# Performance work log

Measured on AMD Instinct MI355X. Metric: run time of the kernel, lower is better.

## Reference

```python
import jax, jax.numpy as jnp
import numpy as np

B, N, FD, D, H, NF, ITERS = 32, 4096, 256, 256, 4, 8, 3
DH = D // H
EPS = 1e-8
SCALE = DH ** -0.5


def layer_norm(x, g, b):
    m = x.mean(-1, keepdims=True)
    v = ((x - m) ** 2).mean(-1, keepdims=True)
    return (x - m) / jnp.sqrt(v + 1e-5) * g + b


def gru_cell(x, h, W_ih, W_hh, b_ih, b_hh):
    # PyTorch GRUCell semantics
    gi = x @ W_ih.T + b_ih  # [n, 3D]
    gh = h @ W_hh.T + b_hh
    ir, iz, inn = jnp.split(gi, 3, axis=-1)
    hr, hz, hn = jnp.split(gh, 3, axis=-1)
    r = jax.nn.sigmoid(ir + hr)
    z = jax.nn.sigmoid(iz + hz)
    n = jnp.tanh(inn + r * hn)
    return (1.0 - z) * n + z * h


def setup_inputs() -> dict:
    key = jax.random.key(0)
    ks = jax.random.split(key, 8)
    s_fd = FD ** -0.5
    s_d = D ** -0.5
    return {
        "inputs": jax.random.normal(ks[0], (B, N, FD), jnp.float32),
        "conditioning": jax.random.normal(ks[1], (B, NF, D), jnp.float32),
        "Wq": jax.random.normal(ks[2], (D, D), jnp.float32) * s_d,
        "Wk": jax.random.normal(ks[3], (D, FD), jnp.float32) * s_fd,
        "Wv": jax.random.normal(ks[4], (D, FD), jnp.float32) * s_fd,
        "W_ih": jax.random.normal(ks[5], (3 * D, D), jnp.float32) * s_d,
        "W_hh": jax.random.normal(ks[6], (3 * D, D), jnp.float32) * s_d,
        "b_ih": jnp.zeros((3 * D,), jnp.float32),
        "b_hh": jnp.zeros((3 * D,), jnp.float32),
        "ln_in_g": jnp.ones((FD,), jnp.float32),
        "ln_in_b": jnp.zeros((FD,), jnp.float32),
        "ln_f_g": jnp.ones((D,), jnp.float32),
        "ln_f_b": jnp.zeros((D,), jnp.float32),
    }


def reference(inputs, conditioning, Wq, Wk, Wv, W_ih, W_hh, b_ih, b_hh,
              ln_in_g, ln_in_b, ln_f_g, ln_f_b):
    b, n, _ = inputs.shape
    nf = conditioning.shape[1]
    x = layer_norm(inputs, ln_in_g, ln_in_b)
    k = (x @ Wk.T).reshape(b, n, H, DH)
    v = (x @ Wv.T).reshape(b, n, H, DH)

    fillers = conditioning
    attn_before = None
    for _ in range(ITERS):
        prev = fillers
        f = layer_norm(fillers, ln_f_g, ln_f_b)
        q = (f @ Wq.T).reshape(b, nf, H, DH)
        dots = jnp.einsum('bihd,bjhd->bihj', q, k) * SCALE  # [b, nf, H, n]
        # inverted softmax: over flattened (slot, head) axis
        attn = jax.nn.softmax(dots.reshape(b, nf * H, n), axis=1).reshape(b, nf, H, n)
        attn_before = attn
        a = attn + EPS
        a = a / a.sum(-1, keepdims=True)
        updates = jnp.einsum('bjhd,bihj->bihd', v, a)  # [b, nf, H, DH]
        fillers = gru_cell(updates.reshape(-1, D), prev.reshape(-1, D),
                           W_ih, W_hh, b_ih, b_hh).reshape(b, nf, D)

    # learnable_roles=False -> roles = identity, so slots == fillers
    slots = fillers
    attn_out = attn_before.mean(axis=2)  # [b, nf, n]
    return slots, attn_out
```

## Files before the change

kernel.cpp:

```cpp
#include <hip/hip_runtime.h>


#define B_ 32
#define N_ 4096
#define H_ 4
#define NF_ 8
#define SH_ 32
#define M_ (B_ * N_)
#define SCALE_ 0.125f
#define EPS_ 1e-8f

typedef __bf16 bf16x8 __attribute__((ext_vector_type(8)));
typedef float f32x4 __attribute__((ext_vector_type(4)));

__device__ __forceinline__ unsigned short f2bf(float f) {
  unsigned int u = __builtin_bit_cast(unsigned int, f);
  u += 0x7fffu + ((u >> 16) & 1u);
  return (unsigned short)(u >> 16);
}
__device__ __forceinline__ float bflo(unsigned int u) {
  return __builtin_bit_cast(float, u << 16);
}
__device__ __forceinline__ float bfhi(unsigned int u) {
  return __builtin_bit_cast(float, u & 0xffff0000u);
}
__device__ __forceinline__ float b2f(unsigned short s) {
  return __builtin_bit_cast(float, ((unsigned int)s) << 16);
}

#define GLDS16(gp, lp)                                                        \
  __builtin_amdgcn_global_load_lds(                                           \
      (const __attribute__((address_space(1))) void*)(gp),                    \
      (__attribute__((address_space(3))) void*)(lp), 16, 0, 0)

__global__ void __launch_bounds__(256) prep_kernel(
    const float* __restrict__ Wq, const float* __restrict__ Wk,
    const float* __restrict__ Wv, const float* __restrict__ Wih,
    const float* __restrict__ Whh, unsigned short* __restrict__ Bkv,
    float* __restrict__ Wqt, unsigned short* __restrict__ Wcat) {
  const int idx = blockIdx.x * 256 + threadIdx.x;
  if (idx < 131072) {
    const int n = idx >> 8, k = idx & 255;
    const float v = (n < 256) ? Wk[n * 256 + k] : Wv[(n - 256) * 256 + k];
    Bkv[idx] = f2bf(v);
  } else if (idx < 196608) {
    const int r = idx - 131072;
    const int k = r >> 8, d = r & 255;
    Wqt[r] = Wq[d * 256 + k];
  } else if (idx < 589824) {
    const int r = idx - 196608;
    const int k = r / 1536, o = r - k * 1536;
    const float v = (o < 768) ? Wih[o * 256 + k] : Whh[(o - 768) * 256 + k];
    Wcat[r] = f2bf(v);
  }
}

__global__ void __launch_bounds__(256) ln_in_kernel(
    const float* __restrict__ in, const float* __restrict__ g,
    const float* __restrict__ bb, unsigned short* __restrict__ x16) {
  const size_t row = (size_t)blockIdx.x * 4 + (threadIdx.x >> 6);
  const int lane = threadIdx.x & 63;
  const float4 xv = *(const float4*)(in + row * 256 + lane * 4);
  float s = xv.x + xv.y + xv.z + xv.w;
  float sq = xv.x * xv.x + xv.y * xv.y + xv.z * xv.z + xv.w * xv.w;
#pragma unroll
  for (int m = 1; m < 64; m <<= 1) {
    s += __shfl_xor(s, m);
    sq += __shfl_xor(sq, m);
  }
  const float mean = s * (1.f / 256.f);
  const float var = sq * (1.f / 256.f) - mean * mean;
  const float rstd = rsqrtf(var + 1e-5f);
  const float4 gv = *(const float4*)(g + lane * 4);
  const float4 bv = *(const float4*)(bb + lane * 4);
  ushort4 o;
  o.x = f2bf((xv.x - mean) * rstd * gv.x + bv.x);
  o.y = f2bf((xv.y - mean) * rstd * gv.y + bv.y);
  o.z = f2bf((xv.z - mean) * rstd * gv.z + bv.z);
  o.w = f2bf((xv.w - mean) * rstd * gv.w + bv.w);
  *(ushort4*)(x16 + row * 256 + lane * 4) = o;
}

__global__ void __launch_bounds__(256) kv_gemm(
    const unsigned short* __restrict__ x16, const unsigned short* __restrict__ Bkv,
    unsigned short* __restrict__ KV) {
  __shared__ __align__(16) unsigned short As[128 * 64];
  __shared__ __align__(16) unsigned short Bs[128 * 64];
  const int m0 = blockIdx.x * 128;
  const int n0 = blockIdx.y * 128;
  const int t = threadIdx.x;
  const int lane = t & 63, wv = t >> 6;
  const int wm = (wv & 1) * 64, wn = (wv >> 1) * 64;
  const int l15 = lane & 15, l4 = lane >> 4;
  f32x4 acc[4][4];
#pragma unroll
  for (int mi = 0; mi < 4; ++mi)
#pragma unroll
    for (int ni = 0; ni < 4; ++ni) {
      acc[mi][ni][0] = 0.f; acc[mi][ni][1] = 0.f;
      acc[mi][ni][2] = 0.f; acc[mi][ni][3] = 0.f;
    }
  const int sr = t >> 3, sc = t & 7;
  for (int kk = 0; kk < 4; ++kk) {
    const int kb = kk * 64;
#pragma unroll
    for (int i = 0; i < 4; ++i) {
      const unsigned short* ga = x16 + (size_t)(m0 + i * 32 + sr) * 256 + kb + sc * 8;
      GLDS16(ga, &As[(i * 32 + sr) * 64 + sc * 8]);
    }
#pragma unroll
    for (int i = 0; i < 4; ++i) {
      const unsigned short* gb = Bkv + (size_t)(n0 + i * 32 + sr) * 256 + kb + sc * 8;
      GLDS16(gb, &Bs[(i * 32 + sr) * 64 + sc * 8]);
    }
    asm volatile("s_waitcnt vmcnt(0)" ::: "memory");
    __syncthreads();
#pragma unroll
    for (int kc = 0; kc < 2; ++kc) {
      bf16x8 af[4], bfr[4];
#pragma unroll
      for (int mi = 0; mi < 4; ++mi)
        af[mi] = *(const bf16x8*)&As[(wm + mi * 16 + l15) * 64 + kc * 32 + l4 * 8];
#pragma unroll
      for (int ni = 0; ni < 4; ++ni)
        bfr[ni] = *(const bf16x8*)&Bs[(wn + ni * 16 + l15) * 64 + kc * 32 + l4 * 8];
#pragma unroll
      for (int mi = 0; mi < 4; ++mi)
#pragma unroll
        for (int ni = 0; ni < 4; ++ni)
          acc[mi][ni] = __builtin_amdgcn_mfma_f32_16x16x32_bf16(
              af[mi], bfr[ni], acc[mi][ni], 0, 0, 0);
    }
    __syncthreads();
  }
#pragma unroll
  for (int mi = 0; mi < 4; ++mi) {
#pragma unroll
    for (int r = 0; r < 4; ++r) {
      const int gm = m0 + wm + mi * 16 + l4 * 4 + r;
      unsigned short* dst = KV + (size_t)gm * 512 + n0 + wn + l15;
#pragma unroll
      for (int ni = 0; ni < 4; ++ni) dst[ni * 16] = f2bf(acc[mi][ni][r]);
    }
  }
}

__global__ void __launch_bounds__(256) qproj_kernel(
    const float* __restrict__ fill, const float* __restrict__ Wqt,
    const float* __restrict__ g, const float* __restrict__ bb,
    float* __restrict__ qbuf) {
  const int bi = blockIdx.x;
  const int t = threadIdx.x;
  const int wv = t >> 6, lane = t & 63;
  __shared__ float f[256];
  __shared__ float red[8];
  const float x = fill[bi * 256 + t];
  float s = x, sq = x * x;
#pragma unroll
  for (int m = 1; m < 64; m <<= 1) {
    s += __shfl_xor(s, m);
    sq += __shfl_xor(sq, m);
  }
  if (lane == 0) {
    red[wv] = s;
    red[4 + wv] = sq;
  }
  __syncthreads();
  const float S = red[0] + red[1] + red[2] + red[3];
  const float SQ = red[4] + red[5] + red[6] + red[7];
  const float mean = S * (1.f / 256.f);
  const float var = SQ * (1.f / 256.f) - mean * mean;
  const float rstd = rsqrtf(var + 1e-5f);
  f[t] = (x - mean) * rstd * g[t] + bb[t];
  __syncthreads();
  float acc = 0.f;
  for (int k = 0; k < 256; ++k) acc = fmaf(f[k], Wqt[k * 256 + t], acc);
  qbuf[(size_t)(bi * 4 + (t >> 6)) * 64 + (t & 63)] = acc;
}

__global__ void __launch_bounds__(256) attn_pass(
    const unsigned short* __restrict__ KV, const float* __restrict__ qbuf,
    float* __restrict__ partials, float* __restrict__ attn_out, int write_attn) {
  const int bid = blockIdx.x;
  const int b = bid >> 5, c = bid & 31;
  const int t = threadIdx.x;
  const int wv = t >> 6, lane = t & 63;
  const int sh = lane & 31, half = lane >> 5;
  const int h = sh & 3;

  float qr[32];
  {
    const float* qp = qbuf + (size_t)(b * 32 + sh) * 64 + half * 32;
#pragma unroll
    for (int x = 0; x < 8; ++x) {
      const float4 v = *(const float4*)(qp + x * 4);
      qr[x * 4 + 0] = v.x; qr[x * 4 + 1] = v.y;
      qr[x * 4 + 2] = v.z; qr[x * 4 + 3] = v.w;
    }
  }
  float upd[32];
#pragma unroll
  for (int x = 0; x < 32; ++x) upd[x] = 0.f;
  float ssum = 0.f;

  const int j0 = c * 128 + wv * 32;
  const unsigned short* rowp = KV + ((size_t)b * N_ + j0) * 512;

  for (int jj = 0; jj < 32; ++jj) {
    const unsigned short* kp = rowp + jj * 512 + h * 64 + half * 32;
    uint4 kw[4], vw[4];
#pragma unroll
    for (int x = 0; x < 4; ++x) kw[x] = *(const uint4*)(kp + x * 8);
#pragma unroll
    for (int x = 0; x < 4; ++x) vw[x] = *(const uint4*)(kp + 256 + x * 8);
    float dot = 0.f;
#pragma unroll
    for (int x = 0; x < 4; ++x) {
      dot = fmaf(qr[x * 8 + 0], bflo(kw[x].x), dot);
      dot = fmaf(qr[x * 8 + 1], bfhi(kw[x].x), dot);
      dot = fmaf(qr[x * 8 + 2], bflo(kw[x].y), dot);
      dot = fmaf(qr[x * 8 + 3], bfhi(kw[x].y), dot);
      dot = fmaf(qr[x * 8 + 4], bflo(kw[x].z), dot);
      dot = fmaf(qr[x * 8 + 5], bfhi(kw[x].z), dot);
      dot = fmaf(qr[x * 8 + 6], bflo(kw[x].w), dot);
      dot = fmaf(qr[x * 8 + 7], bfhi(kw[x].w), dot);
    }
    dot += __shfl_xor(dot, 32);
    const float logit = dot * SCALE_;
    float mx = logit;
#pragma unroll
    for (int m = 1; m <= 16; m <<= 1) mx = fmaxf(mx, __shfl_xor(mx, m));
    const float e = __expf(logit - mx);
    float se = e;
#pragma unroll
    for (int m = 1; m <= 16; m <<= 1) se += __shfl_xor(se, m);
    const float attn = e / se;
    ssum += attn;
#pragma unroll
    for (int x = 0; x < 4; ++x) {
      upd[x * 8 + 0] = fmaf(attn, bflo(vw[x].x), upd[x * 8 + 0]);
      upd[x * 8 + 1] = fmaf(attn, bfhi(vw[x].x), upd[x * 8 + 1]);
      upd[x * 8 + 2] = fmaf(attn, bflo(vw[x].y), upd[x * 8 + 2]);
      upd[x * 8 + 3] = fmaf(attn, bfhi(vw[x].y), upd[x * 8 + 3]);
      upd[x * 8 + 4] = fmaf(attn, bflo(vw[x].z), upd[x * 8 + 4]);
      upd[x * 8 + 5] = fmaf(attn, bfhi(vw[x].z), upd[x * 8 + 5]);
      upd[x * 8 + 6] = fmaf(attn, bflo(vw[x].w), upd[x * 8 + 6]);
      upd[x * 8 + 7] = fmaf(attn, bfhi(vw[x].w), upd[x * 8 + 7]);
    }
    if (write_attn) {
      float hs = attn;
      hs += __shfl_xor(hs, 1);
      hs += __shfl_xor(hs, 2);
      if ((lane & 3) == 0 && half == 0)
        attn_out[((size_t)b * NF_ + (sh >> 2)) * N_ + j0 + jj] = hs * 0.25f;
    }
  }

  __shared__ float uacc[SH_ * 64];
  __shared__ float sacc[SH_];
  for (int x = t; x < SH_ * 64; x += 256) uacc[x] = 0.f;
  if (t < SH_) sacc[t] = 0.f;
  __syncthreads();
  for (int w = 0; w < 4; ++w) {
    if (wv == w) {
#pragma unroll
      for (int x = 0; x < 32; ++x) uacc[sh * 64 + half * 32 + x] += upd[x];
      if (half == 0) sacc[sh] += ssum;
    }
    __syncthreads();
  }
  float* P = partials + (size_t)bid * 2080;
  for (int x = t; x < 2048; x += 256) P[x] = uacc[x];
  if (t < 32) P[2048 + t] = sacc[t];
}

__global__ void __launch_bounds__(256) gru_kernel(
    const float* __restrict__ partials, const float* __restrict__ prev,
    const unsigned short* __restrict__ Wcat, const float* __restrict__ bih,
    const float* __restrict__ bhh, float* __restrict__ out) {
  const int bi = blockIdx.x;
  const int b = bi >> 3;
  const int t = threadIdx.x;
  const int h = t >> 6;
  const int sh = (bi & 7) * 4 + h;
  __shared__ float u[256], pv[256];
  float raw = 0.f, s = 0.f;
  for (int cc = 0; cc < 32; ++cc) {
    const float* Pp = partials + (size_t)(b * 32 + cc) * 2080;
    raw += Pp[sh * 64 + (t & 63)];
    s += Pp[2048 + sh];
  }
  const float uu = raw / (s + (float)N_ * EPS_);
  u[t] = uu;
  pv[t] = prev[bi * 256 + t];
  __syncthreads();
  float a0 = bih[t], a1 = bih[256 + t], a2 = bih[512 + t];
  float a3 = bhh[t], a4 = bhh[256 + t], a5 = bhh[512 + t];
  for (int k = 0; k < 256; ++k) {
    const float uk = u[k], pk = pv[k];
    const unsigned short* wr = Wcat + k * 1536;
    a0 = fmaf(uk, b2f(wr[t]), a0);
    a1 = fmaf(uk, b2f(wr[256 + t]), a1);
    a2 = fmaf(uk, b2f(wr[512 + t]), a2);
    a3 = fmaf(pk, b2f(wr[768 + t]), a3);
    a4 = fmaf(pk, b2f(wr[1024 + t]), a4);
    a5 = fmaf(pk, b2f(wr[1280 + t]), a5);
  }
  const float r = 1.f / (1.f + __expf(-(a0 + a3)));
  const float z = 1.f / (1.f + __expf(-(a1 + a4)));
  const float n = tanhf(a2 + r * a5);
  out[bi * 256 + t] = (1.f - z) * n + z * pv[t];
}

extern "C" void kernel_launch(void* const* d_in, const int* in_sizes, int n_in,
                              void* d_out, int out_size, void* d_ws, size_t ws_size,
                              hipStream_t stream) {
  (void)in_sizes; (void)n_in; (void)out_size; (void)ws_size;
  const float* inputs = (const float*)d_in[0];
  const float* cond = (const float*)d_in[1];
  const float* Wq = (const float*)d_in[2];
  const float* Wk = (const float*)d_in[3];
  const float* Wv = (const float*)d_in[4];
  const float* Wih = (const float*)d_in[5];
  const float* Whh = (const float*)d_in[6];
  const float* bih = (const float*)d_in[7];
  const float* bhh = (const float*)d_in[8];
  const float* lng = (const float*)d_in[9];
  const float* lnb = (const float*)d_in[10];
  const float* lfg = (const float*)d_in[11];
  const float* lfb = (const float*)d_in[12];
  float* out = (float*)d_out;

  char* ws = (char*)d_ws;
  unsigned short* Bkv = (unsigned short*)(ws);
  float* Wqt = (float*)(ws + 262144);
  unsigned short* Wcat = (unsigned short*)(ws + 524288);
  unsigned short* x16 = (unsigned short*)(ws + 1310720);
  unsigned short* KV = (unsigned short*)(ws + 1310720 + 67108864);
  float* qbuf = (float*)(ws + 1310720 + 67108864 + 134217728);
  float* fillA = qbuf + 65536;
  float* fillB = fillA + 65536;
  float* partials = fillB + 65536;

  hipLaunchKernelGGL(prep_kernel, dim3(2304), dim3(256), 0, stream,
                     Wq, Wk, Wv, Wih, Whh, Bkv, Wqt, Wcat);
  hipLaunchKernelGGL(ln_in_kernel, dim3(32768), dim3(256), 0, stream,
                     inputs, lng, lnb, x16);
  hipLaunchKernelGGL(kv_gemm, dim3(1024, 4), dim3(256), 0, stream, x16, Bkv, KV);

  const float* src = cond;
  float* attn_out = out + 65536;
  for (int it = 0; it < 3; ++it) {
    float* dst = (it == 0) ? fillA : (it == 1) ? fillB : out;
    hipLaunchKernelGGL(qproj_kernel, dim3(256), dim3(256), 0, stream,
                       src, Wqt, lfg, lfb, qbuf);
    hipLaunchKernelGGL(attn_pass, dim3(1024), dim3(256), 0, stream,
                       KV, qbuf, partials, attn_out, (it == 2) ? 1 : 0);
    hipLaunchKernelGGL(gru_kernel, dim3(256), dim3(256), 0, stream,
                       partials, src, Wcat, bih, bhh, dst);
    src = dst;
  }
}
```

Before: 776.8 us.

## Compute attention logits with bf16 MFMA using head-masked block-diagonal Q

The qproj kernel now writes Q as bf16 in a zero-padded per-head layout, so each of the 32 slot-head rows spans all 256 key features. The attention pass can then compute all logits for a 32-key chunk with 16x16x32 bf16 MFMA instead of per-lane scalar dot products. Softmax over slot-heads runs on the MFMA accumulator layout, and probabilities are staged as bf16 in padded LDS before the scalar V accumulation. Q and the attention weights lose precision to bf16, and the zero padding does four times the K-dot work. The qtil and fill buffers are moved into the x16 workspace region, which is no longer read after the KV GEMM.

```diff
diff --git a/kernel.cpp b/kernel.cpp
--- a/kernel.cpp
+++ b/kernel.cpp
@@ -6,7 +6,6 @@
 #define H_ 4
 #define NF_ 8
 #define SH_ 32
-#define M_ (B_ * N_)
 #define SCALE_ 0.125f
 #define EPS_ 1e-8f
 
@@ -148,7 +147,7 @@
 __global__ void __launch_bounds__(256) qproj_kernel(
     const float* __restrict__ fill, const float* __restrict__ Wqt,
     const float* __restrict__ g, const float* __restrict__ bb,
-    float* __restrict__ qbuf) {
+    unsigned short* __restrict__ qtil) {
   const int bi = blockIdx.x;
   const int t = threadIdx.x;
   const int wv = t >> 6, lane = t & 63;
@@ -175,103 +174,141 @@
   __syncthreads();
   float acc = 0.f;
   for (int k = 0; k < 256; ++k) acc = fmaf(f[k], Wqt[k * 256 + t], acc);
-  qbuf[(size_t)(bi * 4 + (t >> 6)) * 64 + (t & 63)] = acc;
+  const int b = bi >> 3, i = bi & 7, h = t >> 6;
+  const unsigned short val = f2bf(acc);
+#pragma unroll
+  for (int hp = 0; hp < 4; ++hp)
+    qtil[(size_t)(b * 32 + i * 4 + hp) * 256 + t] = (hp == h) ? val : (unsigned short)0;
 }
 
 __global__ void __launch_bounds__(256) attn_pass(
-    const unsigned short* __restrict__ KV, const float* __restrict__ qbuf,
+    const unsigned short* __restrict__ KV, const unsigned short* __restrict__ qtil,
     float* __restrict__ partials, float* __restrict__ attn_out, int write_attn) {
   const int bid = blockIdx.x;
   const int b = bid >> 5, c = bid & 31;
   const int t = threadIdx.x;
   const int wv = t >> 6, lane = t & 63;
-  const int sh = lane & 31, half = lane >> 5;
-  const int h = sh & 3;
-
-  float qr[32];
-  {
-    const float* qp = qbuf + (size_t)(b * 32 + sh) * 64 + half * 32;
-#pragma unroll
-    for (int x = 0; x < 8; ++x) {
-      const float4 v = *(const float4*)(qp + x * 4);
-      qr[x * 4 + 0] = v.x; qr[x * 4 + 1] = v.y;
-      qr[x * 4 + 2] = v.z; qr[x * 4 + 3] = v.w;
-    }
-  }
+  const int l15 = lane & 15, lq = lane >> 4;
+  const int j0 = c * 128;
+  const int n0 = wv * 32;
+
+  __shared__ unsigned short P[32 * 130];
+  __shared__ float uacc[32 * 65];
+  __shared__ float sred[4 * 32];
+
+  f32x4 acc[2][2];
+#pragma unroll
+  for (int mt = 0; mt < 2; ++mt)
+#pragma unroll
+    for (int nt = 0; nt < 2; ++nt) {
+      acc[mt][nt][0] = 0.f; acc[mt][nt][1] = 0.f;
+      acc[mt][nt][2] = 0.f; acc[mt][nt][3] = 0.f;
+    }
+  const unsigned short* Qb = qtil + (size_t)b * 32 * 256;
+  const unsigned short* Kb = KV + ((size_t)b * N_ + j0 + n0) * 512;
+#pragma unroll
+  for (int ks = 0; ks < 8; ++ks) {
+    const bf16x8 a0 = *(const bf16x8*)(Qb + (size_t)(l15)*256 + ks * 32 + lq * 8);
+    const bf16x8 a1 = *(const bf16x8*)(Qb + (size_t)(16 + l15) * 256 + ks * 32 + lq * 8);
+#pragma unroll
+    for (int nt = 0; nt < 2; ++nt) {
+      const bf16x8 bf = *(const bf16x8*)(Kb + (size_t)(nt * 16 + l15) * 512 + ks * 32 + lq * 8);
+      acc[0][nt] = __builtin_amdgcn_mfma_f32_16x16x32_bf16(a0, bf, acc[0][nt], 0, 0, 0);
+      acc[1][nt] = __builtin_amdgcn_mfma_f32_16x16x32_bf16(a1, bf, acc[1][nt], 0, 0, 0);
+    }
+  }
+
+  float srow[8];
+#pragma unroll
+  for (int i = 0; i < 8; ++i) srow[i] = 0.f;
+#pragma unroll
+  for (int nt = 0; nt < 2; ++nt) {
+    float lv[8];
+#pragma unroll
+    for (int mt = 0; mt < 2; ++mt)
+#pragma unroll
+      for (int r = 0; r < 4; ++r) lv[mt * 4 + r] = acc[mt][nt][r] * SCALE_;
+    float mx = lv[0];
+#pragma unroll
+    for (int i = 1; i < 8; ++i) mx = fmaxf(mx, lv[i]);
+    mx = fmaxf(mx, __shfl_xor(mx, 16));
+    mx = fmaxf(mx, __shfl_xor(mx, 32));
+    float e[8];
+    float cs = 0.f;
+#pragma unroll
+    for (int i = 0; i < 8; ++i) {
+      e[i] = __expf(lv[i] - mx);
+      cs += e[i];
+    }
+    cs += __shfl_xor(cs, 16);
+    cs += __shfl_xor(cs, 32);
+    const float inv = 1.f / cs;
+    const int col = n0 + nt * 16 + l15;
+#pragma unroll
+    for (int mt = 0; mt < 2; ++mt)
+#pragma unroll
+      for (int r = 0; r < 4; ++r) {
+        const float a = e[mt * 4 + r] * inv;
+        srow[mt * 4 + r] += a;
+        P[(mt * 16 + lq * 4 + r) * 130 + col] = f2bf(a);
+      }
+    if (write_attn) {
+#pragma unroll
+      for (int mt = 0; mt < 2; ++mt) {
+        const float ao =
+            (e[mt * 4 + 0] + e[mt * 4 + 1] + e[mt * 4 + 2] + e[mt * 4 + 3]) * inv * 0.25f;
+        attn_out[((size_t)b * NF_ + mt * 4 + lq) * N_ + j0 + col] = ao;
+      }
+    }
+  }
+#pragma unroll
+  for (int k = 1; k <= 8; k <<= 1)
+#pragma unroll
+    for (int i = 0; i < 8; ++i) srow[i] += __shfl_xor(srow[i], k);
+  if (l15 == 0) {
+#pragma unroll
+    for (int mt = 0; mt < 2; ++mt)
+#pragma unroll
+      for (int r = 0; r < 4; ++r)
+        sred[wv * 32 + mt * 16 + lq * 4 + r] = srow[mt * 4 + r];
+  }
+  for (int x = t; x < 32 * 65; x += 256) uacc[x] = 0.f;
+  __syncthreads();
+
+  const int sh = lane & 31, half = lane >> 5, h = sh & 3;
   float upd[32];
 #pragma unroll
   for (int x = 0; x < 32; ++x) upd[x] = 0.f;
-  float ssum = 0.f;
-
-  const int j0 = c * 128 + wv * 32;
-  const unsigned short* rowp = KV + ((size_t)b * N_ + j0) * 512;
-
+  const unsigned short* Vrow =
+      KV + ((size_t)b * N_ + j0 + n0) * 512 + 256 + h * 64 + half * 32;
   for (int jj = 0; jj < 32; ++jj) {
-    const unsigned short* kp = rowp + jj * 512 + h * 64 + half * 32;
-    uint4 kw[4], vw[4];
-#pragma unroll
-    for (int x = 0; x < 4; ++x) kw[x] = *(const uint4*)(kp + x * 8);
-#pragma unroll
-    for (int x = 0; x < 4; ++x) vw[x] = *(const uint4*)(kp + 256 + x * 8);
-    float dot = 0.f;
+    const float a = b2f(P[sh * 130 + n0 + jj]);
+    uint4 vw[4];
+#pragma unroll
+    for (int x = 0; x < 4; ++x) vw[x] = *(const uint4*)(Vrow + jj * 512 + x * 8);
 #pragma unroll
     for (int x = 0; x < 4; ++x) {
-      dot = fmaf(qr[x * 8 + 0], bflo(kw[x].x), dot);
-      dot = fmaf(qr[x * 8 + 1], bfhi(kw[x].x), dot);
-      dot = fmaf(qr[x * 8 + 2], bflo(kw[x].y), dot);
-      dot = fmaf(qr[x * 8 + 3], bfhi(kw[x].y), dot);
-      dot = fmaf(qr[x * 8 + 4], bflo(kw[x].z), dot);
-      dot = fmaf(qr[x * 8 + 5], bfhi(kw[x].z), dot);
-      dot = fmaf(qr[x * 8 + 6], bflo(kw[x].w), dot);
-      dot = fmaf(qr[x * 8 + 7], bfhi(kw[x].w), dot);
-    }
-    dot += __shfl_xor(dot, 32);
-    const float logit = dot * SCALE_;
-    float mx = logit;
-#pragma unroll
-    for (int m = 1; m <= 16; m <<= 1) mx = fmaxf(mx, __shfl_xor(mx, m));
-    const float e = __expf(logit - mx);
-    float se = e;
-#pragma unroll
-    for (int m = 1; m <= 16; m <<= 1) se += __shfl_xor(se, m);
-    const float attn = e / se;
-    ssum += attn;
-#pragma unroll
-    for (int x = 0; x < 4; ++x) {
-      upd[x * 8 + 0] = fmaf(attn, bflo(vw[x].x), upd[x * 8 + 0]);
-      upd[x * 8 + 1] = fmaf(attn, bfhi(vw[x].x), upd[x * 8 + 1]);
-      upd[x * 8 + 2] = fmaf(attn, bflo(vw[x].y), upd[x * 8 + 2]);
-      upd[x * 8 + 3] = fmaf(attn, bfhi(vw[x].y), upd[x * 8 + 3]);
-      upd[x * 8 + 4] = fmaf(attn, bflo(vw[x].z), upd[x * 8 + 4]);
-      upd[x * 8 + 5] = fmaf(attn, bfhi(vw[x].z), upd[x * 8 + 5]);
-      upd[x * 8 + 6] = fmaf(attn, bflo(vw[x].w), upd[x * 8 + 6]);
-      upd[x * 8 + 7] = fmaf(attn, bfhi(vw[x].w), upd[x * 8 + 7]);
-    }
-    if (write_attn) {
-      float hs = attn;
-      hs += __shfl_xor(hs, 1);
-      hs += __shfl_xor(hs, 2);
-      if ((lane & 3) == 0 && half == 0)
-        attn_out[((size_t)b * NF_ + (sh >> 2)) * N_ + j0 + jj] = hs * 0.25f;
-    }
-  }
-
-  __shared__ float uacc[SH_ * 64];
-  __shared__ float sacc[SH_];
-  for (int x = t; x < SH_ * 64; x += 256) uacc[x] = 0.f;
-  if (t < SH_) sacc[t] = 0.f;
-  __syncthreads();
+      upd[x * 8 + 0] = fmaf(a, bflo(vw[x].x), upd[x * 8 + 0]);
+      upd[x * 8 + 1] = fmaf(a, bfhi(vw[x].x), upd[x * 8 + 1]);
+      upd[x * 8 + 2] = fmaf(a, bflo(vw[x].y), upd[x * 8 + 2]);
+      upd[x * 8 + 3] = fmaf(a, bfhi(vw[x].y), upd[x * 8 + 3]);
+      upd[x * 8 + 4] = fmaf(a, bflo(vw[x].z), upd[x * 8 + 4]);
+      upd[x * 8 + 5] = fmaf(a, bfhi(vw[x].z), upd[x * 8 + 5]);
+      upd[x * 8 + 6] = fmaf(a, bflo(vw[x].w), upd[x * 8 + 6]);
+      upd[x * 8 + 7] = fmaf(a, bfhi(vw[x].w), upd[x * 8 + 7]);
+    }
+  }
+
   for (int w = 0; w < 4; ++w) {
     if (wv == w) {
 #pragma unroll
-      for (int x = 0; x < 32; ++x) uacc[sh * 64 + half * 32 + x] += upd[x];
-      if (half == 0) sacc[sh] += ssum;
+      for (int x = 0; x < 32; ++x) uacc[sh * 65 + half * 32 + x] += upd[x];
     }
     __syncthreads();
   }
-  float* P = partials + (size_t)bid * 2080;
-  for (int x = t; x < 2048; x += 256) P[x] = uacc[x];
-  if (t < 32) P[2048 + t] = sacc[t];
+  float* Pp = partials + (size_t)bid * 2080;
+  for (int x = t; x < 2048; x += 256) Pp[x] = uacc[(x >> 6) * 65 + (x & 63)];
+  if (t < 32) Pp[2048 + t] = sred[t] + sred[32 + t] + sred[64 + t] + sred[96 + t];
 }
 
 __global__ void __launch_bounds__(256) gru_kernel(
@@ -337,8 +374,8 @@
   unsigned short* Wcat = (unsigned short*)(ws + 524288);
   unsigned short* x16 = (unsigned short*)(ws + 1310720);
   unsigned short* KV = (unsigned short*)(ws + 1310720 + 67108864);
-  float* qbuf = (float*)(ws + 1310720 + 67108864 + 134217728);
-  float* fillA = qbuf + 65536;
+  unsigned short* qtil = (unsigned short*)(ws + 1310720);
+  float* fillA = (float*)(ws + 1310720 + 524288);
   float* fillB = fillA + 65536;
   float* partials = fillB + 65536;
 
@@ -353,9 +390,9 @@
   for (int it = 0; it < 3; ++it) {
     float* dst = (it == 0) ? fillA : (it == 1) ? fillB : out;
     hipLaunchKernelGGL(qproj_kernel, dim3(256), dim3(256), 0, stream,
-                       src, Wqt, lfg, lfb, qbuf);
+                       src, Wqt, lfg, lfb, qtil);
     hipLaunchKernelGGL(attn_pass, dim3(1024), dim3(256), 0, stream,
-                       KV, qbuf, partials, attn_out, (it == 2) ? 1 : 0);
+                       KV, qtil, partials, attn_out, (it == 2) ? 1 : 0);
     hipLaunchKernelGGL(gru_kernel, dim3(256), dim3(256), 0, stream,
                        partials, src, Wcat, bih, bhh, dst);
     src = dst;
```

After: 632.9 us. -18.5%, faster.
